# Kernel tuning notes

Hardware: AMD Instinct MI355X
Metric: run time of the kernel (lower is better)

The kernel has to match this reference:

```python
import jax, jax.numpy as jnp
import numpy as np

NUM_TAG = 128
T, B = 1024, 512


def setup_inputs() -> dict:
    key = jax.random.key(0)
    k_em, k_tag, k_s, k_t, k_e = jax.random.split(key, 5)
    emissions = jax.random.normal(k_em, (T, B, NUM_TAG), dtype=jnp.float32)
    tags = jax.random.randint(k_tag, (T, B), 0, NUM_TAG, dtype=jnp.int32)
    mask = jnp.ones((T, B), dtype=jnp.float32)
    # parameters: uniform(-0.1, 0.1) as in reset_params
    start_transitions = jax.random.uniform(k_s, (NUM_TAG,), minval=-0.1, maxval=0.1, dtype=jnp.float32)
    transitions = jax.random.uniform(k_t, (NUM_TAG, NUM_TAG), minval=-0.1, maxval=0.1, dtype=jnp.float32)
    end_transitions = jax.random.uniform(k_e, (NUM_TAG,), minval=-0.1, maxval=0.1, dtype=jnp.float32)
    return {
        "emissions": emissions,
        "tags": tags,
        "mask": mask,
        "start_transitions": start_transitions,
        "transitions": transitions,
        "end_transitions": end_transitions,
    }


def _path_score(emissions, tags, mask, start_transitions, transitions, end_transitions):
    # emissions: [T,B,K], tags/mask: [T,B]
    b_idx = jnp.arange(tags.shape[1])
    # emission score of the gold tag at each step: [T,B]
    em_tag = jnp.take_along_axis(emissions, tags[:, :, None].astype(jnp.int32), axis=2)[:, :, 0]
    scores = start_transitions[tags[0]] + (em_tag * mask).sum(axis=0)
    # transition scores along the gold path, masked: [T-1,B]
    scores = scores + (transitions[tags[:-1], tags[1:]] * mask[1:]).sum(axis=0)
    last_idx = mask.astype(jnp.int32).sum(axis=0) - 1  # [B]
    last_tag = tags[last_idx, b_idx]
    return scores + end_transitions[last_tag]


def _log_partition(emissions, mask, start_transitions, transitions, end_transitions):
    log_prob0 = start_transitions[None, :] + emissions[0]  # [B,K]

    def step(log_prob, xs):
        em_t, m_t = xs  # [B,K], [B]
        # score[b,i,j] = log_prob[b,i] + transitions[i,j] + em_t[b,j]
        score = jax.nn.logsumexp(
            log_prob[:, :, None] + transitions[None, :, :] + em_t[:, None, :], axis=1
        )
        new_lp = score * m_t[:, None] + log_prob * (1.0 - m_t)[:, None]
        return new_lp, None

    log_prob, _ = jax.lax.scan(step, log_prob0, (emissions[1:], mask[1:]))
    return jax.nn.logsumexp(log_prob + end_transitions[None, :], axis=1)  # [B]


def reference(emissions, tags, mask, start_transitions, transitions, end_transitions):
    path = _path_score(emissions, tags, mask, start_transitions, transitions, end_transitions)
    log_z = _log_partition(emissions, mask, start_transitions, transitions, end_transitions)
    return (path - log_z).sum()
```

## Files before the change

### kernel.cpp

```cpp
#include <hip/hip_runtime.h>
#include <cstdint>

#define TT 1024
#define BB 512
#define KK 128

__device__ __forceinline__ float rl(float v, int lane) {
  return __uint_as_float((unsigned)__builtin_amdgcn_readlane(__float_as_uint(v), lane));
}

__global__ __launch_bounds__(256, 2) void crf_forward(
    const float* __restrict__ em, const float* __restrict__ mask,
    const float* __restrict__ start_t, const float* __restrict__ trans,
    const float* __restrict__ end_t, float* __restrict__ logz)
{
  const int b    = blockIdx.x;
  const int tid  = threadIdx.x;
  const int lane = tid & 63;
  const int w    = __builtin_amdgcn_readfirstlane(tid >> 6);
  const int c0   = lane * 2;

  __shared__ float smp[2][4][KK];

  float E0[32], E1[32];
#pragma unroll
  for (int ki = 0; ki < 32; ++ki) {
    const float2 tv = *reinterpret_cast<const float2*>(trans + (size_t)(32 * w + ki) * KK + c0);
    E0[ki] = __expf(tv.x);
    E1[ki] = __expf(tv.y);
  }

  const float* em_b = em + (size_t)b * KK + c0;

  float rel0, rel1, p0, p1, base;
  {
    const float2 st = *reinterpret_cast<const float2*>(start_t + c0);
    const float2 e0 = *reinterpret_cast<const float2*>(em_b);
    float nq0 = st.x + e0.x, nq1 = st.y + e0.y;
    float m = fmaxf(nq0, nq1);
#pragma unroll
    for (int off = 32; off; off >>= 1) m = fmaxf(m, __shfl_xor(m, off));
    base = m;
    rel0 = nq0 - m; rel1 = nq1 - m;
    p0 = __expf(rel0); p1 = __expf(rel1);
  }

  float2 em_n = *reinterpret_cast<const float2*>(em_b + (size_t)1 * BB * KK);
  float  mk_n = mask[1 * BB + b];

  for (int t = 1; t < TT; ++t) {
    const int buf = t & 1;
    const float2 em_c = em_n;
    const float  mk_c = mk_n;
    if (t < TT - 1) {
      em_n = *reinterpret_cast<const float2*>(em_b + (size_t)(t + 1) * BB * KK);
      mk_n = mask[(t + 1) * BB + b];
    }

    float a0 = 0.f, a1 = 0.f;
#pragma unroll
    for (int jj = 0; jj < 16; ++jj) {
      const float q0 = rl(p0, 16 * w + jj);
      const float q1 = rl(p1, 16 * w + jj);
      a0 = fmaf(q0, E0[2 * jj], a0);
      a1 = fmaf(q0, E1[2 * jj], a1);
      a0 = fmaf(q1, E0[2 * jj + 1], a0);
      a1 = fmaf(q1, E1[2 * jj + 1], a1);
    }
    *reinterpret_cast<float2*>(&smp[buf][w][c0]) = make_float2(a0, a1);
    __syncthreads();

    const float2 pa = *reinterpret_cast<const float2*>(&smp[buf][0][c0]);
    const float2 pb = *reinterpret_cast<const float2*>(&smp[buf][1][c0]);
    const float2 pc = *reinterpret_cast<const float2*>(&smp[buf][2][c0]);
    const float2 pd = *reinterpret_cast<const float2*>(&smp[buf][3][c0]);
    const float s0 = (pa.x + pb.x) + (pc.x + pd.x);
    const float s1 = (pa.y + pb.y) + (pc.y + pd.y);

    const bool upd = (mk_c != 0.f);
    const float nq0 = upd ? (__logf(s0) + em_c.x) : rel0;
    const float nq1 = upd ? (__logf(s1) + em_c.y) : rel1;

    float m = fmaxf(nq0, nq1);
#pragma unroll
    for (int off = 32; off; off >>= 1) m = fmaxf(m, __shfl_xor(m, off));
    base += m;
    rel0 = nq0 - m; rel1 = nq1 - m;
    p0 = __expf(rel0); p1 = __expf(rel1);
  }

  {
    const float2 ed = *reinterpret_cast<const float2*>(end_t + c0);
    const float v0 = rel0 + ed.x, v1 = rel1 + ed.y;
    float m = fmaxf(v0, v1);
#pragma unroll
    for (int off = 32; off; off >>= 1) m = fmaxf(m, __shfl_xor(m, off));
    float s = __expf(v0 - m) + __expf(v1 - m);
#pragma unroll
    for (int off = 32; off; off >>= 1) s += __shfl_xor(s, off);
    if (tid == 0) logz[b] = base + m + __logf(s);
  }
}

__global__ __launch_bounds__(256) void crf_path(
    const float* __restrict__ em, const int* __restrict__ tags,
    const float* __restrict__ mask, const float* __restrict__ start_t,
    const float* __restrict__ trans, const float* __restrict__ end_t,
    float* __restrict__ path_out)
{
  const int b = blockIdx.x;
  const int tid = threadIdx.x;
  float acc = 0.f, msum = 0.f;
  for (int t = tid; t < TT; t += 256) {
    const int   tg = tags[t * BB + b];
    const float mk = mask[t * BB + b];
    msum += mk;
    acc = fmaf(em[((size_t)t * BB + b) * KK + tg], mk, acc);
    if (t >= 1) {
      const int tgp = tags[(t - 1) * BB + b];
      acc = fmaf(trans[tgp * KK + tg], mk, acc);
    }
  }
  __shared__ float red_a[4], red_m[4];
#pragma unroll
  for (int off = 32; off; off >>= 1) {
    acc  += __shfl_xor(acc, off);
    msum += __shfl_xor(msum, off);
  }
  if ((tid & 63) == 0) { red_a[tid >> 6] = acc; red_m[tid >> 6] = msum; }
  __syncthreads();
  if (tid == 0) {
    float a  = (red_a[0] + red_a[1]) + (red_a[2] + red_a[3]);
    float ms = (red_m[0] + red_m[1]) + (red_m[2] + red_m[3]);
    const int last = (int)(ms + 0.5f) - 1;
    a += start_t[tags[b]] + end_t[tags[(size_t)last * BB + b]];
    path_out[b] = a;
  }
}

__global__ __launch_bounds__(512) void crf_final(
    const float* __restrict__ path, const float* __restrict__ logz,
    float* __restrict__ out)
{
  const int tid = threadIdx.x;
  float v = path[tid] - logz[tid];
  __shared__ float red[8];
#pragma unroll
  for (int off = 32; off; off >>= 1) v += __shfl_xor(v, off);
  if ((tid & 63) == 0) red[tid >> 6] = v;
  __syncthreads();
  if (tid == 0) {
    float s = 0.f;
#pragma unroll
    for (int i = 0; i < 8; ++i) s += red[i];
    out[0] = s;
  }
}

extern "C" void kernel_launch(void* const* d_in, const int* in_sizes, int n_in,
                              void* d_out, int out_size, void* d_ws, size_t ws_size,
                              hipStream_t stream) {
  const float* em    = (const float*)d_in[0];
  const int*   tags  = (const int*)  d_in[1];
  const float* mask  = (const float*)d_in[2];
  const float* st    = (const float*)d_in[3];
  const float* trans = (const float*)d_in[4];
  const float* et    = (const float*)d_in[5];
  float* out = (float*)d_out;

  float* ws_path = (float*)d_ws;
  float* ws_logz = ws_path + BB;

  crf_path   <<<BB, 256, 0, stream>>>(em, tags, mask, st, trans, et, ws_path);
  crf_forward<<<BB, 256, 0, stream>>>(em, mask, st, trans, et, ws_logz);
  crf_final  <<<1, 512, 0, stream>>>(ws_path, ws_logz, out);
}
```

Baseline: 1.296 ms.

## Rewrite CRF forward as batched bf16 MFMA recurrence in linear space

The forward recurrence now processes 16 batch rows per block as a matrix product exp(P)·exp(trans) on bf16 MFMA instructions. It works in linear probability space and rescales by a power of two every four steps instead of taking a log and max-reduce each step. The path score is split into a per-timestep kernel and a per-batch boundary kernel. Only 32 blocks run the serial recurrence, so fewer but heavier blocks occupy the GPU, and the bf16 truncation of probabilities plus the infrequent rescaling risk accuracy loss and overflow or underflow.

```diff
diff --git a/kernel.cpp b/kernel.cpp
--- a/kernel.cpp
+++ b/kernel.cpp
@@ -4,147 +4,223 @@
 #define TT 1024
 #define BB 512
 #define KK 128
-
-__device__ __forceinline__ float rl(float v, int lane) {
-  return __uint_as_float((unsigned)__builtin_amdgcn_readlane(__float_as_uint(v), lane));
-}
-
-__global__ __launch_bounds__(256, 2) void crf_forward(
+#define ST 136
+
+typedef __attribute__((ext_vector_type(8))) short short8;
+typedef __attribute__((ext_vector_type(4))) float f4;
+
+__device__ __forceinline__ unsigned short f2bf_rtne(float x) {
+  unsigned u = __float_as_uint(x);
+  u += 0x7FFF + ((u >> 16) & 1);
+  return (unsigned short)(u >> 16);
+}
+
+__device__ __forceinline__ unsigned pack_trunc(float l, float h) {
+  return __builtin_amdgcn_perm(__float_as_uint(h), __float_as_uint(l), 0x07060302u);
+}
+
+__device__ __forceinline__ void lgkm_barrier() {
+  __atomic_signal_fence(__ATOMIC_SEQ_CST);
+  __builtin_amdgcn_s_waitcnt(0xC07F);
+  __builtin_amdgcn_s_barrier();
+  __atomic_signal_fence(__ATOMIC_SEQ_CST);
+}
+
+__global__ __launch_bounds__(256, 1) void crf_forward(
     const float* __restrict__ em, const float* __restrict__ mask,
     const float* __restrict__ start_t, const float* __restrict__ trans,
     const float* __restrict__ end_t, float* __restrict__ logz)
 {
-  const int b    = blockIdx.x;
   const int tid  = threadIdx.x;
+  const int w    = __builtin_amdgcn_readfirstlane(tid >> 6);
   const int lane = tid & 63;
-  const int w    = __builtin_amdgcn_readfirstlane(tid >> 6);
-  const int c0   = lane * 2;
-
-  __shared__ float smp[2][4][KK];
-
-  float E0[32], E1[32];
-#pragma unroll
-  for (int ki = 0; ki < 32; ++ki) {
-    const float2 tv = *reinterpret_cast<const float2*>(trans + (size_t)(32 * w + ki) * KK + c0);
-    E0[ki] = __expf(tv.x);
-    E1[ki] = __expf(tv.y);
-  }
-
-  const float* em_b = em + (size_t)b * KK + c0;
-
-  float rel0, rel1, p0, p1, base;
+  const int q    = lane >> 4;
+  const int lo   = lane & 15;
+  const int b0   = blockIdx.x * 16;
+
+  __shared__ __align__(16) unsigned short Pt[2][16 * ST];
+  __shared__ __align__(16) float mxs[16][4];
+  __shared__ __align__(16) float psm[16][4];
+
+  const int cb0 = 32 * w + 4 * q;
+  const int cb1 = cb0 + 16;
+
+  const size_t TS = (size_t)BB * KK;
+  const float* emrow = em + (size_t)(b0 + lo) * KK;
+
+  short8 Af[2][4];
+#pragma unroll
+  for (int mti = 0; mti < 2; ++mti) {
+    const int col = 16 * (2 * w + mti) + lo;
+#pragma unroll
+    for (int kt = 0; kt < 4; ++kt) {
+      short8 v;
+#pragma unroll
+      for (int j = 0; j < 8; ++j) {
+        const int k = 32 * kt + 8 * q + j;
+        v[j] = (short)f2bf_rtne(__expf(trans[(size_t)k * KK + col]));
+      }
+      Af[mti][kt] = v;
+    }
+  }
+
+  f4 S0, S1;
+  float base = 0.f;
   {
-    const float2 st = *reinterpret_cast<const float2*>(start_t + c0);
-    const float2 e0 = *reinterpret_cast<const float2*>(em_b);
-    float nq0 = st.x + e0.x, nq1 = st.y + e0.y;
-    float m = fmaxf(nq0, nq1);
-#pragma unroll
-    for (int off = 32; off; off >>= 1) m = fmaxf(m, __shfl_xor(m, off));
-    base = m;
-    rel0 = nq0 - m; rel1 = nq1 - m;
-    p0 = __expf(rel0); p1 = __expf(rel1);
-  }
-
-  float2 em_n = *reinterpret_cast<const float2*>(em_b + (size_t)1 * BB * KK);
-  float  mk_n = mask[1 * BB + b];
+    const f4 e0a = *(const f4*)(emrow + cb0);
+    const f4 e0b = *(const f4*)(emrow + cb1);
+    const f4 st0 = *(const f4*)(start_t + cb0);
+    const f4 st1 = *(const f4*)(start_t + cb1);
+#pragma unroll
+    for (int i = 0; i < 4; ++i) {
+      S0[i] = __expf(st0[i] + e0a[i]);
+      S1[i] = __expf(st1[i] + e0b[i]);
+    }
+    *(uint2*)&Pt[0][lo * ST + cb0] =
+        make_uint2(pack_trunc(S0[0], S0[1]), pack_trunc(S0[2], S0[3]));
+    *(uint2*)&Pt[0][lo * ST + cb1] =
+        make_uint2(pack_trunc(S1[0], S1[1]), pack_trunc(S1[2], S1[3]));
+  }
+
+  f4 eaC = *(const f4*)(emrow + 1 * TS + cb0);
+  f4 ebC = *(const f4*)(emrow + 1 * TS + cb1);
+  f4 eaN = *(const f4*)(emrow + 2 * TS + cb0);
+  f4 ebN = *(const f4*)(emrow + 2 * TS + cb1);
+  float mkC = mask[1 * BB + b0 + lo];
+  float mkN = mask[2 * BB + b0 + lo];
 
   for (int t = 1; t < TT; ++t) {
-    const int buf = t & 1;
-    const float2 em_c = em_n;
-    const float  mk_c = mk_n;
-    if (t < TT - 1) {
-      em_n = *reinterpret_cast<const float2*>(em_b + (size_t)(t + 1) * BB * KK);
-      mk_n = mask[(t + 1) * BB + b];
-    }
-
-    float a0 = 0.f, a1 = 0.f;
-#pragma unroll
-    for (int jj = 0; jj < 16; ++jj) {
-      const float q0 = rl(p0, 16 * w + jj);
-      const float q1 = rl(p1, 16 * w + jj);
-      a0 = fmaf(q0, E0[2 * jj], a0);
-      a1 = fmaf(q0, E1[2 * jj], a1);
-      a0 = fmaf(q1, E0[2 * jj + 1], a0);
-      a1 = fmaf(q1, E1[2 * jj + 1], a1);
-    }
-    *reinterpret_cast<float2*>(&smp[buf][w][c0]) = make_float2(a0, a1);
+    const int pb = (t & 1) ^ 1;
+
+    lgkm_barrier();
+
+    float ps = 1.0f, kln2 = 0.f;
+    const bool scale_step = ((t & 3) == 1) && (t > 1);
+    if (scale_step) {
+      const f4 mv4 = *(const f4*)&mxs[lo][0];
+      const float mv = fmaxf(fmaxf(mv4[0], mv4[1]), fmaxf(mv4[2], mv4[3]));
+      const int k = (int)(__float_as_uint(mv) >> 23) - 127;
+      ps = __uint_as_float((unsigned)(127 - k) << 23);
+      kln2 = (float)k * 0.6931471805599453f;
+    }
+
+    short8 Bf[4];
+#pragma unroll
+    for (int kt = 0; kt < 4; ++kt)
+      Bf[kt] = *(const short8*)&Pt[pb][lo * ST + 32 * kt + 8 * q];
+
+    const int tp = (t + 2 < TT) ? (t + 2) : (TT - 1);
+    const f4 eaL = *(const f4*)(emrow + (size_t)tp * TS + cb0);
+    const f4 ebL = *(const f4*)(emrow + (size_t)tp * TS + cb1);
+    const float mkL = mask[tp * BB + b0 + lo];
+
+    f4 X0, X1;
+#pragma unroll
+    for (int i = 0; i < 4; ++i) { X0[i] = __expf(eaC[i]); X1[i] = __expf(ebC[i]); }
+    if (scale_step) { X0 *= ps; X1 *= ps; }
+
+    f4 a0 = {0.f, 0.f, 0.f, 0.f}, a1 = {0.f, 0.f, 0.f, 0.f};
+#pragma unroll
+    for (int kt = 0; kt < 4; ++kt) {
+      a0 = __builtin_amdgcn_mfma_f32_16x16x32_bf16(Af[0][kt], Bf[kt], a0, 0, 0, 0);
+      a1 = __builtin_amdgcn_mfma_f32_16x16x32_bf16(Af[1][kt], Bf[kt], a1, 0, 0, 0);
+    }
+
+    const bool upd = (mkC != 0.f);
+#pragma unroll
+    for (int i = 0; i < 4; ++i) {
+      const float n0 = a0[i] * X0[i];
+      const float n1 = a1[i] * X1[i];
+      S0[i] = upd ? n0 : S0[i];
+      S1[i] = upd ? n1 : S1[i];
+    }
+    if (scale_step && upd) base += kln2;
+
+    *(uint2*)&Pt[t & 1][lo * ST + cb0] =
+        make_uint2(pack_trunc(S0[0], S0[1]), pack_trunc(S0[2], S0[3]));
+    *(uint2*)&Pt[t & 1][lo * ST + cb1] =
+        make_uint2(pack_trunc(S1[0], S1[1]), pack_trunc(S1[2], S1[3]));
+
+    if ((t & 3) == 0) {
+      float mv = fmaxf(fmaxf(fmaxf(S0[0], S0[1]), fmaxf(S0[2], S0[3])),
+                       fmaxf(fmaxf(S1[0], S1[1]), fmaxf(S1[2], S1[3])));
+      mv = fmaxf(mv, __shfl_xor(mv, 16));
+      mv = fmaxf(mv, __shfl_xor(mv, 32));
+      if (q == 0) mxs[lo][w] = mv;
+    }
+
+    eaC = eaN; ebC = ebN; eaN = eaL; ebN = ebL;
+    mkC = mkN; mkN = mkL;
+  }
+
+  {
+    const f4 ed0 = *(const f4*)(end_t + cb0);
+    const f4 ed1 = *(const f4*)(end_t + cb1);
+    float s = 0.f;
+#pragma unroll
+    for (int i = 0; i < 4; ++i)
+      s += S0[i] * __expf(ed0[i]) + S1[i] * __expf(ed1[i]);
+    s += __shfl_xor(s, 16);
+    s += __shfl_xor(s, 32);
+    if (q == 0) psm[lo][w] = s;
     __syncthreads();
-
-    const float2 pa = *reinterpret_cast<const float2*>(&smp[buf][0][c0]);
-    const float2 pb = *reinterpret_cast<const float2*>(&smp[buf][1][c0]);
-    const float2 pc = *reinterpret_cast<const float2*>(&smp[buf][2][c0]);
-    const float2 pd = *reinterpret_cast<const float2*>(&smp[buf][3][c0]);
-    const float s0 = (pa.x + pb.x) + (pc.x + pd.x);
-    const float s1 = (pa.y + pb.y) + (pc.y + pd.y);
-
-    const bool upd = (mk_c != 0.f);
-    const float nq0 = upd ? (__logf(s0) + em_c.x) : rel0;
-    const float nq1 = upd ? (__logf(s1) + em_c.y) : rel1;
-
-    float m = fmaxf(nq0, nq1);
-#pragma unroll
-    for (int off = 32; off; off >>= 1) m = fmaxf(m, __shfl_xor(m, off));
-    base += m;
-    rel0 = nq0 - m; rel1 = nq1 - m;
-    p0 = __expf(rel0); p1 = __expf(rel1);
-  }
-
-  {
-    const float2 ed = *reinterpret_cast<const float2*>(end_t + c0);
-    const float v0 = rel0 + ed.x, v1 = rel1 + ed.y;
-    float m = fmaxf(v0, v1);
-#pragma unroll
-    for (int off = 32; off; off >>= 1) m = fmaxf(m, __shfl_xor(m, off));
-    float s = __expf(v0 - m) + __expf(v1 - m);
-#pragma unroll
-    for (int off = 32; off; off >>= 1) s += __shfl_xor(s, off);
-    if (tid == 0) logz[b] = base + m + __logf(s);
-  }
-}
-
-__global__ __launch_bounds__(256) void crf_path(
+    if (tid < 16) {
+      const f4 pv = *(const f4*)&psm[tid][0];
+      logz[b0 + tid] = base + logf(pv[0] + pv[1] + pv[2] + pv[3]);
+    }
+  }
+}
+
+__global__ __launch_bounds__(512) void crf_path_tb(
     const float* __restrict__ em, const int* __restrict__ tags,
-    const float* __restrict__ mask, const float* __restrict__ start_t,
-    const float* __restrict__ trans, const float* __restrict__ end_t,
-    float* __restrict__ path_out)
-{
-  const int b = blockIdx.x;
+    const float* __restrict__ mask, const float* __restrict__ trans,
+    float* __restrict__ ws_tb)
+{
+  const int t = blockIdx.x, b = threadIdx.x;
+  const int tg = tags[t * BB + b];
+  const float mk = mask[t * BB + b];
+  float v = em[((size_t)t * BB + b) * KK + tg] * mk;
+  if (t >= 1) {
+    const int tgp = tags[(t - 1) * BB + b];
+    v += trans[(size_t)tgp * KK + tg] * mk;
+  }
+  __shared__ float red[8];
+#pragma unroll
+  for (int off = 32; off; off >>= 1) v += __shfl_xor(v, off);
+  if ((b & 63) == 0) red[b >> 6] = v;
+  __syncthreads();
+  if (b == 0) {
+    float s = 0.f;
+#pragma unroll
+    for (int i = 0; i < 8; ++i) s += red[i];
+    ws_tb[t] = s;
+  }
+}
+
+__global__ __launch_bounds__(64) void crf_bterm(
+    const int* __restrict__ tags, const float* __restrict__ mask,
+    const float* __restrict__ start_t, const float* __restrict__ end_t,
+    float* __restrict__ ws_bt)
+{
+  const int b = blockIdx.x, tid = threadIdx.x;
+  float ms = 0.f;
+  for (int t = tid; t < TT; t += 64) ms += mask[t * BB + b];
+#pragma unroll
+  for (int off = 32; off; off >>= 1) ms += __shfl_xor(ms, off);
+  if (tid == 0) {
+    const int last = (int)(ms + 0.5f) - 1;
+    ws_bt[b] = start_t[tags[b]] + end_t[tags[(size_t)last * BB + b]];
+  }
+}
+
+__global__ __launch_bounds__(1024) void crf_final(
+    const float* __restrict__ ws_tb, const float* __restrict__ ws_bt,
+    const float* __restrict__ ws_lz, float* __restrict__ out)
+{
   const int tid = threadIdx.x;
-  float acc = 0.f, msum = 0.f;
-  for (int t = tid; t < TT; t += 256) {
-    const int   tg = tags[t * BB + b];
-    const float mk = mask[t * BB + b];
-    msum += mk;
-    acc = fmaf(em[((size_t)t * BB + b) * KK + tg], mk, acc);
-    if (t >= 1) {
-      const int tgp = tags[(t - 1) * BB + b];
-      acc = fmaf(trans[tgp * KK + tg], mk, acc);
-    }
-  }
-  __shared__ float red_a[4], red_m[4];
-#pragma unroll
-  for (int off = 32; off; off >>= 1) {
-    acc  += __shfl_xor(acc, off);
-    msum += __shfl_xor(msum, off);
-  }
-  if ((tid & 63) == 0) { red_a[tid >> 6] = acc; red_m[tid >> 6] = msum; }
-  __syncthreads();
-  if (tid == 0) {
-    float a  = (red_a[0] + red_a[1]) + (red_a[2] + red_a[3]);
-    float ms = (red_m[0] + red_m[1]) + (red_m[2] + red_m[3]);
-    const int last = (int)(ms + 0.5f) - 1;
-    a += start_t[tags[b]] + end_t[tags[(size_t)last * BB + b]];
-    path_out[b] = a;
-  }
-}
-
-__global__ __launch_bounds__(512) void crf_final(
-    const float* __restrict__ path, const float* __restrict__ logz,
-    float* __restrict__ out)
-{
-  const int tid = threadIdx.x;
-  float v = path[tid] - logz[tid];
-  __shared__ float red[8];
+  float v = ws_tb[tid];
+  if (tid < BB) v += ws_bt[tid] - ws_lz[tid];
+  __shared__ float red[16];
 #pragma unroll
   for (int off = 32; off; off >>= 1) v += __shfl_xor(v, off);
   if ((tid & 63) == 0) red[tid >> 6] = v;
@@ -152,7 +228,7 @@
   if (tid == 0) {
     float s = 0.f;
 #pragma unroll
-    for (int i = 0; i < 8; ++i) s += red[i];
+    for (int i = 0; i < 16; ++i) s += red[i];
     out[0] = s;
   }
 }
@@ -160,6 +236,7 @@
 extern "C" void kernel_launch(void* const* d_in, const int* in_sizes, int n_in,
                               void* d_out, int out_size, void* d_ws, size_t ws_size,
                               hipStream_t stream) {
+  (void)in_sizes; (void)n_in; (void)out_size; (void)ws_size;
   const float* em    = (const float*)d_in[0];
   const int*   tags  = (const int*)  d_in[1];
   const float* mask  = (const float*)d_in[2];
@@ -168,10 +245,12 @@
   const float* et    = (const float*)d_in[5];
   float* out = (float*)d_out;
 
-  float* ws_path = (float*)d_ws;
-  float* ws_logz = ws_path + BB;
-
-  crf_path   <<<BB, 256, 0, stream>>>(em, tags, mask, st, trans, et, ws_path);
-  crf_forward<<<BB, 256, 0, stream>>>(em, mask, st, trans, et, ws_logz);
-  crf_final  <<<1, 512, 0, stream>>>(ws_path, ws_logz, out);
-}
+  float* ws_tb = (float*)d_ws;
+  float* ws_bt = ws_tb + 1024;
+  float* ws_lz = ws_bt + 512;
+
+  crf_path_tb<<<TT, 512, 0, stream>>>(em, tags, mask, trans, ws_tb);
+  crf_bterm  <<<BB, 64, 0, stream>>>(tags, mask, st, et, ws_bt);
+  crf_forward<<<32, 256, 0, stream>>>(em, mask, st, trans, et, ws_lz);
+  crf_final  <<<1, 1024, 0, stream>>>(ws_tb, ws_bt, ws_lz, out);
+}
```

Result: faster. 1.114 ms (-14.1%).
